# Performance work log

Hardware: AMD Instinct MI355X
Metric: run time of the kernel (lower is better)

Reference implementation:

```python
import jax, jax.numpy as jnp
import numpy as np

H = 128  # LSTM hidden size
EPS = 1e-5  # BatchNorm eps


def _lstm_scan(seq, Wih, Whh, bih, bhh, h0, c0):
    """Unbatched LSTM over seq [N, D] with torch gate order (i, f, g, o)."""
    b = bih + bhh

    def step(carry, xt):
        h, c = carry
        gates = xt @ Wih.T + h @ Whh.T + b  # [4H]
        i, f, g, o = jnp.split(gates, 4)
        i = jax.nn.sigmoid(i)
        f = jax.nn.sigmoid(f)
        g = jnp.tanh(g)
        o = jax.nn.sigmoid(o)
        c = f * c + i * g
        h = o * jnp.tanh(c)
        return (h, c), h

    (h, c), ys = jax.lax.scan(step, (h0, c0), seq)
    return ys  # [N, H]


def _lstm_forward(x, Wih, Whh, bih, bhh, h0, c0):
    # Faithful to TypeNet.lstm_forward: for each timestep i, x[:, i] ([B, D])
    # is fed to nn.LSTM as an UNBATCHED sequence of length B, and the final
    # (hx, cx) carries into the next timestep column. This is equivalent to a
    # single scan over the flattened [T*B, D] sequence (column-major order).
    B, T, D = x.shape
    seq = jnp.transpose(x, (1, 0, 2)).reshape(T * B, D)
    ys = _lstm_scan(seq, Wih, Whh, bih, bhh, h0, c0)
    return ys.reshape(T, B, H)  # matches torch.stack(output, dim=0)


def _bn(x, gamma, beta):
    # BatchNorm1d in training-mode math over (N, C, L): stats over dims (0, 2).
    mean = x.mean(axis=(0, 2), keepdims=True)
    var = ((x - mean) ** 2).mean(axis=(0, 2), keepdims=True)
    return gamma[None, :, None] * (x - mean) * jax.lax.rsqrt(var + EPS) + beta[None, :, None]


def _single_forward(x, branch, g1, b1, Wih1, Whh1, bih1, bhh1,
                    g2, b2, Wih2, Whh2, bih2, bhh2, h0s, c0s):
    x = _bn(x, g1, b1)                                        # [128, 16, 3]
    x = _lstm_forward(x, Wih1, Whh1, bih1, bhh1,
                      h0s[2 * branch], c0s[2 * branch])       # [16, 128, 128]
    # dropout layers are identity (p = 0.0)
    x = _bn(x, g2, b2)                                        # C = 128 at dim 1
    x = _lstm_forward(x, Wih2, Whh2, bih2, bhh2,
                      h0s[2 * branch + 1], c0s[2 * branch + 1])  # [128, 16, 128]
    return x


def setup_inputs() -> dict:
    key = jax.random.key(0)
    ks = jax.random.split(key, 12)
    s = 1.0 / np.sqrt(H)  # torch LSTM init scale
    return {
        "x": jax.random.normal(ks[0], (128, 48, 3), dtype=jnp.float32),
        "g1": jnp.ones((16,), jnp.float32),
        "b1": jnp.zeros((16,), jnp.float32),
        "Wih1": jax.random.uniform(ks[1], (4 * H, 3), jnp.float32, -s, s),
        "Whh1": jax.random.uniform(ks[2], (4 * H, H), jnp.float32, -s, s),
        "bih1": jax.random.uniform(ks[3], (4 * H,), jnp.float32, -s, s),
        "bhh1": jax.random.uniform(ks[4], (4 * H,), jnp.float32, -s, s),
        "g2": jnp.ones((H,), jnp.float32),
        "b2": jnp.zeros((H,), jnp.float32),
        "Wih2": jax.random.uniform(ks[5], (4 * H, H), jnp.float32, -s, s),
        "Whh2": jax.random.uniform(ks[6], (4 * H, H), jnp.float32, -s, s),
        "bih2": jax.random.uniform(ks[7], (4 * H,), jnp.float32, -s, s),
        "bhh2": jax.random.uniform(ks[8], (4 * H,), jnp.float32, -s, s),
        # 6 LSTM calls (2 layers x 3 branches), each with its own random init state
        "h0s": jax.random.normal(ks[9], (6, H), dtype=jnp.float32),
        "c0s": jax.random.normal(ks[10], (6, H), dtype=jnp.float32),
    }


def reference(x, g1, b1, Wih1, Whh1, bih1, bhh1,
              g2, b2, Wih2, Whh2, bih2, bhh2, h0s, c0s):
    d1, d2, d3 = jnp.split(x, 3, axis=1)  # each [128, 16, 3]
    args = (g1, b1, Wih1, Whh1, bih1, bhh1, g2, b2, Wih2, Whh2, bih2, bhh2, h0s, c0s)
    anchor = _single_forward(d1, 0, *args)
    positive = _single_forward(d2, 1, *args)
    negative = _single_forward(d3, 2, *args)
    return anchor, positive, negative  # each [128, 16, 128]
```

## Files before the change

### kernel.cpp

```cpp
#include <hip/hip_runtime.h>


typedef _Float16 half4_t __attribute__((ext_vector_type(4)));
typedef _Float16 half8 __attribute__((ext_vector_type(8)));
typedef float float4_t __attribute__((ext_vector_type(4)));

#define LOG2E 1.44269504f

__device__ __forceinline__ float fast_rcp(float x) { return __builtin_amdgcn_rcpf(x); }
__device__ __forceinline__ float exp2b(float x) { return __builtin_amdgcn_exp2f(x); }

#define QBCAST(x, pat)                                                        \
  __int_as_float(__builtin_amdgcn_update_dpp(0, __float_as_int(x), (pat),     \
                                             0xF, 0xF, true))

__device__ __forceinline__ void lds_barrier() {
  asm volatile("s_waitcnt lgkmcnt(0)\n\ts_barrier" ::: "memory");
}

__host__ __device__ __forceinline__ int ridx0_of(int j) {
  return (j >> 4) * 64 + ((j >> 2) & 3) * 16 + (j & 3) * 4;
}

__global__ __launch_bounds__(128) void bn1_kernel(const float* __restrict__ x,
                                                  const float* __restrict__ g1,
                                                  const float* __restrict__ b1,
                                                  float* __restrict__ xbn) {
  const int br = blockIdx.x >> 4;
  const int t  = blockIdx.x & 15;
  const int b  = threadIdx.x;
  const float* px = x + (b * 48 + br * 16 + t) * 3;
  const float v0 = px[0], v1 = px[1], v2 = px[2];
  float s  = v0 + v1 + v2;
  float ss = v0 * v0 + v1 * v1 + v2 * v2;
  for (int off = 32; off; off >>= 1) {
    s  += __shfl_down(s, off);
    ss += __shfl_down(ss, off);
  }
  __shared__ float red[4];
  if ((threadIdx.x & 63) == 0) {
    red[(threadIdx.x >> 6) * 2]     = s;
    red[(threadIdx.x >> 6) * 2 + 1] = ss;
  }
  __syncthreads();
  const float S = red[0] + red[2], SS = red[1] + red[3];
  const float mean = S * (1.0f / 384.0f);
  const float var  = SS * (1.0f / 384.0f) - mean * mean;
  const float rstd = rsqrtf(var + 1e-5f);
  const float a  = g1[t] * rstd;
  const float sh = b1[t] - mean * a;
  float* dst = xbn + br * 6144 + (t * 128 + b) * 3;
  dst[0] = v0 * a + sh;
  dst[1] = v1 * a + sh;
  dst[2] = v2 * a + sh;
}

__global__ __launch_bounds__(256) void g1x_kernel(const float* __restrict__ xbn,
                                                  const float* __restrict__ Wih1,
                                                  const float* __restrict__ bih1,
                                                  const float* __restrict__ bhh1,
                                                  _Float16* __restrict__ G1x) {
  const int br = blockIdx.x >> 10;
  const int sp = blockIdx.x & 1023;
  const int s  = sp * 2 + (threadIdx.x >> 7);
  const int j  = threadIdx.x & 127;
  const float* px = xbn + br * 6144 + s * 3;
  const float x0 = px[0], x1 = px[1], x2 = px[2];
  _Float16* base =
      G1x + ((size_t)(br * 128 + (s >> 4)) * 512 + ridx0_of(j)) * 16 + (s & 15);
#pragma unroll
  for (int g = 0; g < 4; ++g) {
    const int row = g * 128 + j;
    const float a = bih1[row] + bhh1[row] + Wih1[row * 3] * x0 +
                    Wih1[row * 3 + 1] * x1 + Wih1[row * 3 + 2] * x2;
    base[g * 16] = (_Float16)(a * LOG2E);
  }
}

__global__ __launch_bounds__(256) void bn2stats_kernel(const float* __restrict__ H1,
                                                       float* __restrict__ stats) {
  const int br = blockIdx.x >> 7;
  const int ch = blockIdx.x & 127;
  const float* base = H1 + (size_t)br * 262144 + ch * 128;
  float s = 0.f, ss = 0.f;
  for (int k = threadIdx.x; k < 2048; k += 256) {
    const int t1 = k >> 7, h = k & 127;
    const float v = base[t1 * 16384 + h];
    s += v;
    ss += v * v;
  }
  for (int off = 32; off; off >>= 1) {
    s  += __shfl_down(s, off);
    ss += __shfl_down(ss, off);
  }
  __shared__ float red[8];
  if ((threadIdx.x & 63) == 0) {
    red[(threadIdx.x >> 6) * 2]     = s;
    red[(threadIdx.x >> 6) * 2 + 1] = ss;
  }
  __syncthreads();
  if (threadIdx.x == 0) {
    const float S  = red[0] + red[2] + red[4] + red[6];
    const float SS = red[1] + red[3] + red[5] + red[7];
    const float mean = S * (1.0f / 2048.0f);
    const float var  = SS * (1.0f / 2048.0f) - mean * mean;
    stats[(br * 128 + ch) * 2]     = mean;
    stats[(br * 128 + ch) * 2 + 1] = rsqrtf(var + 1e-5f);
  }
}

__global__ __launch_bounds__(256) void g2x_kernel(
    const float* __restrict__ H1, const float* __restrict__ stats,
    const float* __restrict__ g2, const float* __restrict__ b2v,
    const float* __restrict__ Wih2, const float* __restrict__ bih2,
    const float* __restrict__ bhh2, _Float16* __restrict__ G2x) {
  const int br = blockIdx.x >> 7;
  const int t2 = blockIdx.x & 127;
  __shared__ float xh[2048];
  __shared__ float wt[64 * 129];
  const float mean = stats[(br * 128 + t2) * 2];
  const float rstd = stats[(br * 128 + t2) * 2 + 1];
  const float a  = g2[t2] * rstd;
  const float sh = b2v[t2] - mean * a;
  for (int e = threadIdx.x; e < 2048; e += 256) {
    const int b2 = e >> 7, d = e & 127;
    xh[e] = H1[(size_t)br * 262144 + (size_t)(b2 * 128 + t2) * 128 + d] * a + sh;
  }
  const int gl  = threadIdx.x & 63;
  const int b2b = (threadIdx.x >> 6) * 4;
  for (int gt = 0; gt < 8; ++gt) {
    __syncthreads();
    for (int e = threadIdx.x; e < 8192; e += 256)
      wt[(e >> 7) * 129 + (e & 127)] = Wih2[gt * 8192 + e];
    __syncthreads();
    float a0 = 0.f, a1 = 0.f, a2 = 0.f, a3 = 0.f;
    for (int d = 0; d < 128; ++d) {
      const float w = wt[gl * 129 + d];
      a0 += w * xh[(b2b + 0) * 128 + d];
      a1 += w * xh[(b2b + 1) * 128 + d];
      a2 += w * xh[(b2b + 2) * 128 + d];
      a3 += w * xh[(b2b + 3) * 128 + d];
    }
    const int g    = gt * 64 + gl;
    const int gate = g >> 7;
    const int jj   = g & 127;
    const int ri   = ridx0_of(jj) + gate;
    const float bb = bih2[g] + bhh2[g];
    _Float16* dst = G2x + ((size_t)(br * 128 + t2) * 512 + ri) * 16 + b2b;
    *reinterpret_cast<half4_t*>(dst) =
        half4_t{(_Float16)((a0 + bb) * LOG2E), (_Float16)((a1 + bb) * LOG2E),
                (_Float16)((a2 + bb) * LOG2E), (_Float16)((a3 + bb) * LOG2E)};
  }
}

__global__ __launch_bounds__(512, 1) void lstm_kernel(
    const float* __restrict__ Whh, const float* __restrict__ h0s,
    const float* __restrict__ c0s, const _Float16* __restrict__ Gx,
    float* __restrict__ outp, int layer) {
  const int br   = blockIdx.x;
  const int tid  = threadIdx.x;
  const int wave = tid >> 6;
  const int lane = tid & 63;
  const int quad = lane >> 4;
  const int l15  = lane & 15;
  const int gate = l15 & 3;
  const int rr   = l15 >> 2;
  const int j    = wave * 16 + quad * 4 + rr;
  const bool rb0 = (rr & 1) != 0;
  const bool rb1 = (rr & 2) != 0;
  const bool gb0 = (gate & 1) != 0;
  const bool gb1 = (gate & 2) != 0;
  const float sc = (gate == 2) ? 2.0f : 1.0f;
  const float Bc = (gate == 2) ? 2.0f : 1.0f;

  __shared__ __align__(16) _Float16 h_sh[2][128];

  half8 afrag[4][4];
#pragma unroll
  for (int g = 0; g < 4; ++g) {
    const int row = g * 128 + wave * 16 + l15;
#pragma unroll
    for (int kt = 0; kt < 4; ++kt) {
      const float* src = Whh + row * 128 + kt * 32 + quad * 8;
      half8 f;
#pragma unroll
      for (int jj = 0; jj < 8; ++jj) f[jj] = (_Float16)(src[jj] * LOG2E);
      afrag[g][kt] = f;
    }
  }

  const int slot = 2 * br + layer;
  float c = c0s[slot * 128 + j];
  if (tid < 128) h_sh[0][tid] = (_Float16)h0s[slot * 128 + tid];

  const half8* gq = (const half8*)Gx;
  half8 curA = gq[((size_t)(br * 128) * 512 + tid) * 2];
  half8 curB = gq[((size_t)(br * 128) * 512 + tid) * 2 + 1];
  float* op = outp + (size_t)br * 262144 + j;

  const float4_t zacc = {0.f, 0.f, 0.f, 0.f};
  __syncthreads();

  for (int chk = 0; chk < 128; ++chk) {
    const int chn = (chk < 127) ? chk + 1 : 127;
    const size_t nrec = ((size_t)(br * 128 + chn) * 512 + tid) * 2;
    const half8 nA = gq[nrec], nB = gq[nrec + 1];

#pragma unroll
    for (int u = 0; u < 16; ++u) {
      const _Float16* hcur = h_sh[u & 1];
      half8 bfrag[4];
#pragma unroll
      for (int kt = 0; kt < 4; ++kt)
        bfrag[kt] = *reinterpret_cast<const half8*>(&hcur[kt * 32 + quad * 8]);

      const float pre = (float)((u < 8) ? curA[u] : curB[u - 8]);

      float4_t acc[4];
#pragma unroll
      for (int g = 0; g < 4; ++g)
        acc[g] = __builtin_amdgcn_mfma_f32_16x16x32_f16(afrag[g][0], bfrag[0],
                                                        zacc, 0, 0, 0);
#pragma unroll
      for (int kt = 1; kt < 4; ++kt)
#pragma unroll
        for (int g = 0; g < 4; ++g)
          acc[g] = __builtin_amdgcn_mfma_f32_16x16x32_f16(afrag[g][kt],
                                                          bfrag[kt], acc[g], 0, 0, 0);

      float e0, e1, e2, e3;
      {
        float x, y;
        x = rb0 ? acc[0][1] : acc[0][0]; y = rb0 ? acc[0][3] : acc[0][2];
        e0 = rb1 ? y : x;
        x = rb0 ? acc[1][1] : acc[1][0]; y = rb0 ? acc[1][3] : acc[1][2];
        e1 = rb1 ? y : x;
        x = rb0 ? acc[2][1] : acc[2][0]; y = rb0 ? acc[2][3] : acc[2][2];
        e2 = rb1 ? y : x;
        x = rb0 ? acc[3][1] : acc[3][0]; y = rb0 ? acc[3][3] : acc[3][2];
        e3 = rb1 ? y : x;
      }
      const float eA = gb0 ? e1 : e0;
      const float eB = gb0 ? e3 : e2;
      const float a  = (gb1 ? eB : eA) + pre;

      const float act = __builtin_fmaf(-Bc, fast_rcp(1.0f + exp2b(sc * a)), 1.0f);

      const float iv = QBCAST(act, 0x00);
      const float fv = QBCAST(act, 0x55);
      const float gv = QBCAST(act, 0xAA);
      const float ov = QBCAST(act, 0xFF);

      c = fv * c + iv * gv;
      const float t  = __builtin_fmaf(
          -2.0f, fast_rcp(1.0f + exp2b(c * 2.88539008f)), 1.0f);
      const float hv = ov * t;

      if (gate == 0) {
        h_sh[(u + 1) & 1][j] = (_Float16)hv;
        *op = hv;
      }
      op += 128;
      lds_barrier();
    }

    curA = nA;
    curB = nB;
  }
}

extern "C" void kernel_launch(void* const* d_in, const int* in_sizes, int n_in,
                              void* d_out, int out_size, void* d_ws, size_t ws_size,
                              hipStream_t stream) {
  const float* x    = (const float*)d_in[0];
  const float* g1   = (const float*)d_in[1];
  const float* b1   = (const float*)d_in[2];
  const float* Wih1 = (const float*)d_in[3];
  const float* Whh1 = (const float*)d_in[4];
  const float* bih1 = (const float*)d_in[5];
  const float* bhh1 = (const float*)d_in[6];
  const float* g2   = (const float*)d_in[7];
  const float* b2   = (const float*)d_in[8];
  const float* Wih2 = (const float*)d_in[9];
  const float* Whh2 = (const float*)d_in[10];
  const float* bih2 = (const float*)d_in[11];
  const float* bhh2 = (const float*)d_in[12];
  const float* h0s  = (const float*)d_in[13];
  const float* c0s  = (const float*)d_in[14];

  float* ws   = (float*)d_ws;
  float* xbn  = ws;
  float* H1b  = ws + 18432;
  float* st   = ws + 18432 + 786432;
  _Float16* G1xb = (_Float16*)(ws + 805632);
  _Float16* G2xb = (_Float16*)(ws + 2378496);
  float* outp = (float*)d_out;

  bn1_kernel<<<48, 128, 0, stream>>>(x, g1, b1, xbn);
  g1x_kernel<<<3072, 256, 0, stream>>>(xbn, Wih1, bih1, bhh1, G1xb);
  lstm_kernel<<<3, 512, 0, stream>>>(Whh1, h0s, c0s, G1xb, H1b, 0);
  bn2stats_kernel<<<384, 256, 0, stream>>>(H1b, st);
  g2x_kernel<<<384, 256, 0, stream>>>(H1b, st, g2, b2, Wih2, bih2, bhh2, G2xb);
  lstm_kernel<<<3, 512, 0, stream>>>(Whh2, h0s, c0s, G2xb, outp, 1);
}
```

Before: 1.856 ms.

## Spread LSTM recurrence over 16 waves with per-lane gate activations

The recurrent LSTM kernel moves from 8 to 16 waves per block. Each wave now handles 8 hidden units and issues 8 MFMAs per step instead of 16, and each lane computes all four gate activations itself, so the DPP quad broadcasts and the gate-select logic are gone. The precomputed input-gate buffers switch to a layout with 8-step chunks and all four gates adjacent per hidden unit, to match the new lane mapping. The aim is to shorten the serial per-step critical path. In exchange every step now needs a barrier across 16 waves, each lane does more transcendental work, and most lanes compute redundant results.

```diff
diff --git a/kernel.cpp b/kernel.cpp
--- a/kernel.cpp
+++ b/kernel.cpp
@@ -10,17 +10,10 @@
 __device__ __forceinline__ float fast_rcp(float x) { return __builtin_amdgcn_rcpf(x); }
 __device__ __forceinline__ float exp2b(float x) { return __builtin_amdgcn_exp2f(x); }
 
-#define QBCAST(x, pat)                                                        \
-  __int_as_float(__builtin_amdgcn_update_dpp(0, __float_as_int(x), (pat),     \
-                                             0xF, 0xF, true))
-
 __device__ __forceinline__ void lds_barrier() {
   asm volatile("s_waitcnt lgkmcnt(0)\n\ts_barrier" ::: "memory");
 }
 
-__host__ __device__ __forceinline__ int ridx0_of(int j) {
-  return (j >> 4) * 64 + ((j >> 2) & 3) * 16 + (j & 3) * 4;
-}
 
 __global__ __launch_bounds__(128) void bn1_kernel(const float* __restrict__ x,
                                                   const float* __restrict__ g1,
@@ -67,13 +60,13 @@
   const float* px = xbn + br * 6144 + s * 3;
   const float x0 = px[0], x1 = px[1], x2 = px[2];
   _Float16* base =
-      G1x + ((size_t)(br * 128 + (s >> 4)) * 512 + ridx0_of(j)) * 16 + (s & 15);
+      G1x + (((size_t)(br * 256 + (s >> 3)) * 128 + j) * 4) * 8 + (s & 7);
 #pragma unroll
   for (int g = 0; g < 4; ++g) {
     const int row = g * 128 + j;
     const float a = bih1[row] + bhh1[row] + Wih1[row * 3] * x0 +
                     Wih1[row * 3 + 1] * x1 + Wih1[row * 3 + 2] * x2;
-    base[g * 16] = (_Float16)(a * LOG2E);
+    base[g * 8] = (_Float16)(a * LOG2E);
   }
 }
 
@@ -144,16 +137,17 @@
     const int g    = gt * 64 + gl;
     const int gate = g >> 7;
     const int jj   = g & 127;
-    const int ri   = ridx0_of(jj) + gate;
     const float bb = bih2[g] + bhh2[g];
-    _Float16* dst = G2x + ((size_t)(br * 128 + t2) * 512 + ri) * 16 + b2b;
+    _Float16* dst =
+        G2x + (((size_t)(br * 256 + t2 * 2 + (b2b >> 3)) * 128 + jj) * 4 + gate) * 8 +
+        (b2b & 7);
     *reinterpret_cast<half4_t*>(dst) =
         half4_t{(_Float16)((a0 + bb) * LOG2E), (_Float16)((a1 + bb) * LOG2E),
                 (_Float16)((a2 + bb) * LOG2E), (_Float16)((a3 + bb) * LOG2E)};
   }
 }
 
-__global__ __launch_bounds__(512, 1) void lstm_kernel(
+__global__ __launch_bounds__(1024, 4) void lstm_kernel(
     const float* __restrict__ Whh, const float* __restrict__ h0s,
     const float* __restrict__ c0s, const _Float16* __restrict__ Gx,
     float* __restrict__ outp, int layer) {
@@ -163,29 +157,27 @@
   const int lane = tid & 63;
   const int quad = lane >> 4;
   const int l15  = lane & 15;
-  const int gate = l15 & 3;
-  const int rr   = l15 >> 2;
-  const int j    = wave * 16 + quad * 4 + rr;
-  const bool rb0 = (rr & 1) != 0;
-  const bool rb1 = (rr & 2) != 0;
-  const bool gb0 = (gate & 1) != 0;
-  const bool gb1 = (gate & 2) != 0;
-  const float sc = (gate == 2) ? 2.0f : 1.0f;
-  const float Bc = (gate == 2) ? 2.0f : 1.0f;
+  const int jp   = l15 & 1;
+  const int j    = wave * 8 + 2 * quad + jp;
+  const bool store = (l15 < 2);
 
   __shared__ __align__(16) _Float16 h_sh[2][128];
 
-  half8 afrag[4][4];
-#pragma unroll
-  for (int g = 0; g < 4; ++g) {
-    const int row = g * 128 + wave * 16 + l15;
-#pragma unroll
-    for (int kt = 0; kt < 4; ++kt) {
-      const float* src = Whh + row * 128 + kt * 32 + quad * 8;
-      half8 f;
-#pragma unroll
-      for (int jj = 0; jj < 8; ++jj) f[jj] = (_Float16)(src[jj] * LOG2E);
-      afrag[g][kt] = f;
+  half8 afrag[2][4];
+  {
+    const int rg = (l15 >> 1) & 1;
+    const int rj = wave * 8 + 2 * (l15 >> 2) + (l15 & 1);
+#pragma unroll
+    for (int t = 0; t < 2; ++t) {
+      const int row = (t * 2 + rg) * 128 + rj;
+#pragma unroll
+      for (int kt = 0; kt < 4; ++kt) {
+        const float* src = Whh + row * 128 + kt * 32 + quad * 8;
+        half8 f;
+#pragma unroll
+        for (int jj = 0; jj < 8; ++jj) f[jj] = (_Float16)(src[jj] * LOG2E);
+        afrag[t][kt] = f;
+      }
     }
   }
 
@@ -194,69 +186,58 @@
   if (tid < 128) h_sh[0][tid] = (_Float16)h0s[slot * 128 + tid];
 
   const half8* gq = (const half8*)Gx;
-  half8 curA = gq[((size_t)(br * 128) * 512 + tid) * 2];
-  half8 curB = gq[((size_t)(br * 128) * 512 + tid) * 2 + 1];
+  size_t gb = ((size_t)(br * 256) * 128 + j) * 4;
+  half8 cur0 = gq[gb], cur1 = gq[gb + 1], cur2 = gq[gb + 2], cur3 = gq[gb + 3];
   float* op = outp + (size_t)br * 262144 + j;
 
   const float4_t zacc = {0.f, 0.f, 0.f, 0.f};
   __syncthreads();
 
-  for (int chk = 0; chk < 128; ++chk) {
-    const int chn = (chk < 127) ? chk + 1 : 127;
-    const size_t nrec = ((size_t)(br * 128 + chn) * 512 + tid) * 2;
-    const half8 nA = gq[nrec], nB = gq[nrec + 1];
-
-#pragma unroll
-    for (int u = 0; u < 16; ++u) {
+  for (int ch = 0; ch < 256; ++ch) {
+    const int chn = (ch < 255) ? ch + 1 : 255;
+    const size_t nb = ((size_t)(br * 256 + chn) * 128 + j) * 4;
+    const half8 n0 = gq[nb], n1 = gq[nb + 1], n2 = gq[nb + 2], n3 = gq[nb + 3];
+
+#pragma unroll
+    for (int u = 0; u < 8; ++u) {
       const _Float16* hcur = h_sh[u & 1];
       half8 bfrag[4];
 #pragma unroll
       for (int kt = 0; kt < 4; ++kt)
         bfrag[kt] = *reinterpret_cast<const half8*>(&hcur[kt * 32 + quad * 8]);
 
-      const float pre = (float)((u < 8) ? curA[u] : curB[u - 8]);
-
-      float4_t acc[4];
-#pragma unroll
-      for (int g = 0; g < 4; ++g)
-        acc[g] = __builtin_amdgcn_mfma_f32_16x16x32_f16(afrag[g][0], bfrag[0],
-                                                        zacc, 0, 0, 0);
-#pragma unroll
-      for (int kt = 1; kt < 4; ++kt)
-#pragma unroll
-        for (int g = 0; g < 4; ++g)
-          acc[g] = __builtin_amdgcn_mfma_f32_16x16x32_f16(afrag[g][kt],
-                                                          bfrag[kt], acc[g], 0, 0, 0);
-
-      float e0, e1, e2, e3;
-      {
-        float x, y;
-        x = rb0 ? acc[0][1] : acc[0][0]; y = rb0 ? acc[0][3] : acc[0][2];
-        e0 = rb1 ? y : x;
-        x = rb0 ? acc[1][1] : acc[1][0]; y = rb0 ? acc[1][3] : acc[1][2];
-        e1 = rb1 ? y : x;
-        x = rb0 ? acc[2][1] : acc[2][0]; y = rb0 ? acc[2][3] : acc[2][2];
-        e2 = rb1 ? y : x;
-        x = rb0 ? acc[3][1] : acc[3][0]; y = rb0 ? acc[3][3] : acc[3][2];
-        e3 = rb1 ? y : x;
+      float4_t acc0 = __builtin_amdgcn_mfma_f32_16x16x32_f16(afrag[0][0], bfrag[0],
+                                                             zacc, 0, 0, 0);
+      float4_t acc1 = __builtin_amdgcn_mfma_f32_16x16x32_f16(afrag[1][0], bfrag[0],
+                                                             zacc, 0, 0, 0);
+#pragma unroll
+      for (int kt = 1; kt < 4; ++kt) {
+        acc0 = __builtin_amdgcn_mfma_f32_16x16x32_f16(afrag[0][kt], bfrag[kt],
+                                                      acc0, 0, 0, 0);
+        acc1 = __builtin_amdgcn_mfma_f32_16x16x32_f16(afrag[1][kt], bfrag[kt],
+                                                      acc1, 0, 0, 0);
       }
-      const float eA = gb0 ? e1 : e0;
-      const float eB = gb0 ? e3 : e2;
-      const float a  = (gb1 ? eB : eA) + pre;
-
-      const float act = __builtin_fmaf(-Bc, fast_rcp(1.0f + exp2b(sc * a)), 1.0f);
-
-      const float iv = QBCAST(act, 0x00);
-      const float fv = QBCAST(act, 0x55);
-      const float gv = QBCAST(act, 0xAA);
-      const float ov = QBCAST(act, 0xFF);
-
+
+      const float p0 = (float)cur0[u];
+      const float p1 = (float)cur1[u];
+      const float p2 = (float)cur2[u];
+      const float p3 = (float)cur3[u];
+
+      const float gi = (jp ? acc0[1] : acc0[0]) + p0;
+      const float gf = (jp ? acc0[3] : acc0[2]) + p1;
+      const float gg = (jp ? acc1[1] : acc1[0]) + p2;
+      const float go = (jp ? acc1[3] : acc1[2]) + p3;
+
+      const float iv = fast_rcp(1.0f + exp2b(-gi));
+      const float fv = fast_rcp(1.0f + exp2b(-gf));
+      const float gv = __builtin_fmaf(-2.0f, fast_rcp(1.0f + exp2b(gg + gg)), 1.0f);
+      const float ov = fast_rcp(1.0f + exp2b(-go));
       c = fv * c + iv * gv;
       const float t  = __builtin_fmaf(
           -2.0f, fast_rcp(1.0f + exp2b(c * 2.88539008f)), 1.0f);
       const float hv = ov * t;
 
-      if (gate == 0) {
+      if (store) {
         h_sh[(u + 1) & 1][j] = (_Float16)hv;
         *op = hv;
       }
@@ -264,8 +245,7 @@
       lds_barrier();
     }
 
-    curA = nA;
-    curB = nB;
+    cur0 = n0; cur1 = n1; cur2 = n2; cur3 = n3;
   }
 }
 
@@ -298,8 +278,8 @@
 
   bn1_kernel<<<48, 128, 0, stream>>>(x, g1, b1, xbn);
   g1x_kernel<<<3072, 256, 0, stream>>>(xbn, Wih1, bih1, bhh1, G1xb);
-  lstm_kernel<<<3, 512, 0, stream>>>(Whh1, h0s, c0s, G1xb, H1b, 0);
+  lstm_kernel<<<3, 1024, 0, stream>>>(Whh1, h0s, c0s, G1xb, H1b, 0);
   bn2stats_kernel<<<384, 256, 0, stream>>>(H1b, st);
   g2x_kernel<<<384, 256, 0, stream>>>(H1b, st, g2, b2, Wih2, bih2, bhh2, G2xb);
-  lstm_kernel<<<3, 512, 0, stream>>>(Whh2, h0s, c0s, G2xb, outp, 1);
-}
+  lstm_kernel<<<3, 1024, 0, stream>>>(Whh2, h0s, c0s, G2xb, outp, 1);
+}
```

Result: slower. 2.363 ms (+27.3%).
